# Kernel tuning notes

Hardware: AMD Instinct MI355X
Metric: run time of the kernel (lower is better)

The kernel has to match this reference:

```python
import jax, jax.numpy as jnp
import numpy as np
import math

B, T, D, H = 2, 2048, 1024, 16
HD = D // H  # head_dim = 64
ROPE_BASE = 10000.0


def _rope_tables(t_len, dim, base, dtype=jnp.float32):
    inv_freq = 1.0 / (base ** (jnp.arange(0, dim, 2, dtype=jnp.float32) / dim))
    t = jnp.arange(t_len, dtype=jnp.float32)
    freqs = jnp.outer(t, inv_freq)                 # [T, dim/2]
    emb = jnp.concatenate([freqs, freqs], axis=-1)  # [T, dim]
    return jnp.cos(emb).astype(dtype), jnp.sin(emb).astype(dtype)


def _rotate_half(x):
    x1, x2 = jnp.split(x, 2, axis=-1)
    return jnp.concatenate([-x2, x1], axis=-1)


def _apply_rotary(x, cos, sin):
    # x: [B,H,T,hd]; cos/sin: [T,hd] broadcast over B,H
    return x * cos[None, None, :, :] + _rotate_half(x) * sin[None, None, :, :]


def setup_inputs() -> dict:
    key = jax.random.key(0)
    ks = jax.random.split(key, 5)
    x = jax.random.normal(ks[0], (B, T, D), dtype=jnp.float32)
    Wq = jax.random.normal(ks[1], (D, D), dtype=jnp.float32) * (1.0 / math.sqrt(D))
    Wk = jax.random.normal(ks[2], (D, D), dtype=jnp.float32) * (1.0 / math.sqrt(D))
    Wv = jax.random.normal(ks[3], (D, D), dtype=jnp.float32) * (1.0 / math.sqrt(D))
    Wo = jax.random.normal(ks[4], (D, D), dtype=jnp.float32) * (1.0 / math.sqrt(D))
    # additive causal mask: 0 on/below diagonal, -inf above
    neg = jnp.finfo(jnp.float32).min
    mask = jnp.where(jnp.tril(jnp.ones((T, T), dtype=bool)), 0.0, neg).astype(jnp.float32)
    return {"x": x, "mask": mask, "Wq": Wq, "Wk": Wk, "Wv": Wv, "Wo": Wo}


def reference(x, mask, Wq, Wk, Wv, Wo):
    scale = math.sqrt(HD)
    # projections (nn.Linear: y = x @ W.T), split heads -> [B,H,T,hd]
    q = jnp.einsum('btd,ed->bte', x, Wq).reshape(B, T, H, HD).transpose(0, 2, 1, 3)
    k = jnp.einsum('btd,ed->bte', x, Wk).reshape(B, T, H, HD).transpose(0, 2, 1, 3)
    v = jnp.einsum('btd,ed->bte', x, Wv).reshape(B, T, H, HD).transpose(0, 2, 1, 3)
    cos, sin = _rope_tables(T, HD, ROPE_BASE, x.dtype)
    q = _apply_rotary(q, cos, sin)
    k = _apply_rotary(k, cos, sin)
    scores = jnp.einsum('bhqd,bhkd->bhqk', q, k) / scale   # [B,H,T,T]
    scores = scores + mask[None, None, :, :]
    attn_weights = jax.nn.softmax(scores, axis=-1)          # [B,H,T,T]
    # dropout=0.0 (eval): attn_weights_dropped == attn_weights
    out = jnp.einsum('bhqk,bhkd->bhqd', attn_weights, v)    # [B,H,T,hd]
    out = out.transpose(0, 2, 1, 3).reshape(B, T, D)
    out = jnp.einsum('btd,ed->bte', out, Wo)
    return out, attn_weights
```

## Files before the change

### kernel.cpp

```cpp
#include <hip/hip_runtime.h>
#include <math.h>

#define Tn 2048
#define Dn 1024
#define Hn 16
#define HDn 64

typedef float f32x4 __attribute__((ext_vector_type(4)));
typedef _Float16 f16x8 __attribute__((ext_vector_type(8)));
typedef _Float16 f16x4 __attribute__((ext_vector_type(4)));
typedef __fp16 fp16x2 __attribute__((ext_vector_type(2)));

__device__ __forceinline__ f32x4 mfma16(f16x8 a, f16x8 b, f32x4 c) {
  return __builtin_amdgcn_mfma_f32_16x16x32_f16(a, b, c, 0, 0, 0);
}

__device__ __forceinline__ void cvt_store4(_Float16* dst, float4 v) {
  union { _Float16 h[4]; uint2 u; } pk;
  pk.h[0] = (_Float16)v.x; pk.h[1] = (_Float16)v.y;
  pk.h[2] = (_Float16)v.z; pk.h[3] = (_Float16)v.w;
  *reinterpret_cast<uint2*>(dst) = pk.u;
}

__device__ __forceinline__ void nt_store4v(float* p, f32x4 t) {
  __builtin_nontemporal_store(t, reinterpret_cast<f32x4*>(p));
}

__device__ __forceinline__ f16x4 pk4(float a, float b, float c, float d) {
  union { fp16x2 v[2]; f16x4 h; } u;
  u.v[0] = __builtin_amdgcn_cvt_pkrtz(a, b);
  u.v[1] = __builtin_amdgcn_cvt_pkrtz(c, d);
  return u.h;
}

#define SOFT_SYNC do {                                        \
    __builtin_amdgcn_sched_barrier(0);                        \
    asm volatile("s_waitcnt lgkmcnt(0)" ::: "memory");        \
    __builtin_amdgcn_s_barrier();                             \
    __builtin_amdgcn_sched_barrier(0);                        \
  } while (0)

__global__ __launch_bounds__(256) void cvt_fp16_kernel(
    const float* __restrict__ x, const float* __restrict__ wq,
    const float* __restrict__ wk, const float* __restrict__ wv,
    const float* __restrict__ wo,
    _Float16* __restrict__ xh, _Float16* __restrict__ wqh,
    _Float16* __restrict__ wkh, _Float16* __restrict__ wvh,
    _Float16* __restrict__ woh)
{
  int i = blockIdx.x * 256 + threadIdx.x;
  const float* src; _Float16* dst; int off;
  if (i < 1048576) { src = x; dst = xh; off = i; }
  else {
    int j = i - 1048576;
    int w = j >> 18; off = j & 262143;
    src = (w == 0) ? wq : (w == 1) ? wk : (w == 2) ? wv : wo;
    dst = (w == 0) ? wqh : (w == 1) ? wkh : (w == 2) ? wvh : woh;
  }
  float4 v = reinterpret_cast<const float4*>(src)[off];
  cvt_store4(dst + (size_t)off * 4, v);
}

__global__ void rope_table_kernel(float* __restrict__ cosT, float* __restrict__ sinT) {
  int i = blockIdx.x * 256 + threadIdx.x;
  if (i >= Tn * 32) return;
  int t = i >> 5, f = i & 31;
  float inv = powf(10000.0f, -(float)(2 * f) / 64.0f);
  float ang = (float)t * inv;
  float c = cosf(ang), s = sinf(ang);
  cosT[t * HDn + f] = c; cosT[t * HDn + f + 32] = c;
  sinT[t * HDn + f] = s; sinT[t * HDn + f + 32] = s;
}

__global__ __launch_bounds__(256) void proj_kernel(
    const _Float16* __restrict__ xh, const _Float16* __restrict__ wqh,
    const _Float16* __restrict__ wkh, const _Float16* __restrict__ wvh,
    const float* __restrict__ cosT, const float* __restrict__ sinT,
    _Float16* __restrict__ qh, _Float16* __restrict__ kh, _Float16* __restrict__ vh)
{
  const int w = blockIdx.z;
  const _Float16* __restrict__ W = (w == 0) ? wqh : (w == 1) ? wkh : wvh;
  _Float16* __restrict__ dst = (w == 0) ? qh : (w == 1) ? kh : vh;
  __shared__ _Float16 As[128][72];
  __shared__ _Float16 Bs[128][72];
  const int tid = threadIdx.x;
  const int lane = tid & 63, wave = tid >> 6;
  const int lrow = lane & 15, lhi = lane >> 4;
  const int wm = wave >> 1, wn = wave & 1;
  const int m0 = blockIdx.x * 128, n0 = blockIdx.y * 128;
  f32x4 acc[4][4];
#pragma unroll
  for (int i = 0; i < 4; ++i)
#pragma unroll
    for (int j = 0; j < 4; ++j) acc[i][j] = f32x4{0.f, 0.f, 0.f, 0.f};

  for (int k0 = 0; k0 < Dn; k0 += 64) {
#pragma unroll
    for (int it = 0; it < 4; ++it) {
      int idx = it * 2048 + tid * 8;
      int r = idx >> 6, c = idx & 63;
      *reinterpret_cast<uint4*>(&As[r][c]) =
          *reinterpret_cast<const uint4*>(xh + (size_t)(m0 + r) * Dn + k0 + c);
      *reinterpret_cast<uint4*>(&Bs[r][c]) =
          *reinterpret_cast<const uint4*>(W + (size_t)(n0 + r) * Dn + k0 + c);
    }
    __syncthreads();
#pragma unroll
    for (int kc = 0; kc < 2; ++kc) {
      f16x8 af[4], bf[4];
#pragma unroll
      for (int i = 0; i < 4; ++i)
        af[i] = *reinterpret_cast<const f16x8*>(&As[wm * 64 + i * 16 + lrow][kc * 32 + lhi * 8]);
#pragma unroll
      for (int j = 0; j < 4; ++j)
        bf[j] = *reinterpret_cast<const f16x8*>(&Bs[wn * 64 + j * 16 + lrow][kc * 32 + lhi * 8]);
#pragma unroll
      for (int i = 0; i < 4; ++i)
#pragma unroll
        for (int j = 0; j < 4; ++j)
          acc[i][j] = mfma16(af[i], bf[j], acc[i][j]);
    }
    __syncthreads();
  }
  const bool isqk = (w < 2);
#pragma unroll
  for (int i = 0; i < 4; ++i) {
#pragma unroll
    for (int r = 0; r < 4; ++r) {
      int rowg = m0 + wm * 64 + i * 16 + lhi * 4 + r;
      int bb = rowg >> 11, t = rowg & (Tn - 1);
#pragma unroll
      for (int j = 0; j < 4; ++j) {
        int colg = n0 + wn * 64 + j * 16 + lrow;
        int hh = colg >> 6, d = colg & 63;
        float val = acc[i][j][r];
        if (isqk) {
          float partner = acc[i][j ^ 2][r];
          float rot = (j < 2) ? -partner : partner;
          val = val * cosT[t * HDn + d] + rot * sinT[t * HDn + d];
        }
        dst[(((size_t)(bb * Hn + hh)) * Tn + t) * HDn + d] = (_Float16)val;
      }
    }
  }
}

__global__ __launch_bounds__(256) void attn_kernel(
    const _Float16* __restrict__ qh, const _Float16* __restrict__ kh,
    const _Float16* __restrict__ vh, float* __restrict__ attnw,
    _Float16* __restrict__ obuf)
{
  const int f = blockIdx.x;
  const int s = f >> 3, g = s >> 5;
  const int my_bh = (f & 7) + 8 * g;
  const int c = ((s & 31) + 8 * g) & 31;
  const int b = my_bh >> 4, h = my_bh & 15;
  const size_t bh = (size_t)my_bh;
  const _Float16* __restrict__ Qp = qh + bh * Tn * HDn;
  const _Float16* __restrict__ Kp = kh + bh * Tn * HDn;
  const _Float16* __restrict__ Vp = vh + bh * Tn * HDn;
  float* __restrict__ attnp = attnw + bh * (size_t)Tn * Tn;

  __shared__ _Float16 Ks[128][72];
  __shared__ _Float16 Vt[64][136];
  __shared__ _Float16 Pt[4][16][136];

  const int tid = threadIdx.x;
  const int lane = tid & 63, wave = tid >> 6;
  const int q16 = lane & 15, lhi = lane >> 4;
  const int qp0 = c * 64;
  const int wrow = qp0 + wave * 16;
  const int qg = wrow + q16;
  const int ntiles = (c >> 1) + 1;

  f16x8 bq[2];
#pragma unroll
  for (int kc = 0; kc < 2; ++kc) {
    bq[kc] = *reinterpret_cast<const f16x8*>(
        Qp + (size_t)qg * HDn + kc * 32 + lhi * 8);
    bq[kc] = bq[kc] * (_Float16)0.18033688f;
  }

  float lsum = 0.f;
  for (int kt = 0; kt < ntiles; ++kt) {
#pragma unroll
    for (int it = 0; it < 4; ++it) {
      int idx = it * 2048 + tid * 8;
      int r = idx >> 6, cc = idx & 63;
      *reinterpret_cast<uint4*>(&Ks[r][cc]) =
          *reinterpret_cast<const uint4*>(Kp + (size_t)(kt * 128 + r) * HDn + cc);
    }
    SOFT_SYNC;
    f32x4 st[8];
#pragma unroll
    for (int nf = 0; nf < 8; ++nf) st[nf] = f32x4{0.f, 0.f, 0.f, 0.f};
#pragma unroll
    for (int kc = 0; kc < 2; ++kc) {
      f16x8 ak[8];
#pragma unroll
      for (int nf = 0; nf < 8; ++nf)
        ak[nf] = *reinterpret_cast<const f16x8*>(&Ks[nf * 16 + q16][kc * 32 + lhi * 8]);
#pragma unroll
      for (int nf = 0; nf < 8; ++nf) st[nf] = mfma16(ak[nf], bq[kc], st[nf]);
    }
    const bool diag = (kt == ntiles - 1);
#pragma unroll
    for (int nf = 0; nf < 8; ++nf) {
      int kbase = kt * 128 + nf * 16 + lhi * 4;
#pragma unroll
      for (int r = 0; r < 4; ++r) {
        float v = st[nf][r];
        if (diag && (kbase + r) > qg) v = -INFINITY;
        lsum += __builtin_amdgcn_exp2f(v);
      }
    }
    SOFT_SYNC;
  }
  lsum += __shfl_xor(lsum, 16);
  lsum += __shfl_xor(lsum, 32);
  const float lg = __builtin_amdgcn_logf(lsum);

  f32x4 oacc[4];
#pragma unroll
  for (int df = 0; df < 4; ++df) oacc[df] = f32x4{0.f, 0.f, 0.f, 0.f};

  for (int kt = 0; kt < ntiles; ++kt) {
#pragma unroll
    for (int it = 0; it < 4; ++it) {
      int idx = it * 2048 + tid * 8;
      int r = idx >> 6, cc = idx & 63;
      *reinterpret_cast<uint4*>(&Ks[r][cc]) =
          *reinterpret_cast<const uint4*>(Kp + (size_t)(kt * 128 + r) * HDn + cc);
      uint4 vv = *reinterpret_cast<const uint4*>(Vp + (size_t)(kt * 128 + r) * HDn + cc);
      const _Float16* pv = reinterpret_cast<const _Float16*>(&vv);
      int colb = ((((r >> 3) ^ (cc >> 3)) & 15) << 3) | (r & 7);
#pragma unroll
      for (int j = 0; j < 8; ++j) Vt[cc + j][colb] = pv[j];
    }
    SOFT_SYNC;
    f32x4 st[8];
#pragma unroll
    for (int nf = 0; nf < 8; ++nf) st[nf] = f32x4{0.f, 0.f, 0.f, 0.f};
#pragma unroll
    for (int kc = 0; kc < 2; ++kc) {
      f16x8 ak[8];
#pragma unroll
      for (int nf = 0; nf < 8; ++nf)
        ak[nf] = *reinterpret_cast<const f16x8*>(&Ks[nf * 16 + q16][kc * 32 + lhi * 8]);
#pragma unroll
      for (int nf = 0; nf < 8; ++nf) st[nf] = mfma16(ak[nf], bq[kc], st[nf]);
    }
    const bool diag = (kt == ntiles - 1);
#pragma unroll
    for (int nf = 0; nf < 8; ++nf) {
      int kbase = kt * 128 + nf * 16 + lhi * 4;
      float p[4];
#pragma unroll
      for (int r = 0; r < 4; ++r) {
        float v = st[nf][r];
        if (diag && (kbase + r) > qg) v = -INFINITY;
        p[r] = __builtin_amdgcn_exp2f(v - lg);
      }
      *reinterpret_cast<f16x4*>(&Pt[wave][q16][nf * 16 + lhi * 4]) =
          pk4(p[0], p[1], p[2], p[3]);
    }
#pragma unroll
    for (int kc2 = 0; kc2 < 4; ++kc2) {
      f16x8 ap = *reinterpret_cast<const f16x8*>(&Pt[wave][q16][kc2 * 32 + lhi * 8]);
      f16x8 bv[4];
#pragma unroll
      for (int df = 0; df < 4; ++df) {
        int d = df * 16 + q16;
        int colb = (((4 * kc2 + lhi) ^ ((d >> 3) & 7)) & 15) << 3;
        bv[df] = *reinterpret_cast<const f16x8*>(&Vt[d][colb]);
      }
#pragma unroll
      for (int df = 0; df < 4; ++df) oacc[df] = mfma16(ap, bv[df], oacc[df]);
    }
    {
      const int qrd = (lane >> 5);
      const int k4 = (lane & 31) * 4;
#pragma unroll
      for (int it2 = 0; it2 < 8; ++it2) {
        int qrow = it2 * 2 + qrd;
        f16x4 ph = *reinterpret_cast<const f16x4*>(&Pt[wave][qrow][k4]);
        f32x4 pf;
        pf[0] = (float)ph[0]; pf[1] = (float)ph[1];
        pf[2] = (float)ph[2]; pf[3] = (float)ph[3];
        nt_store4v(attnp + (size_t)(wrow + qrow) * Tn + kt * 128 + k4, pf);
      }
    }
    SOFT_SYNC;
  }

#pragma unroll
  for (int df = 0; df < 4; ++df)
#pragma unroll
    for (int r = 0; r < 4; ++r)
      obuf[((size_t)(b * Tn + wrow + lhi * 4 + r)) * Dn + h * HDn + df * 16 + q16] =
          (_Float16)oacc[df][r];

  int zc0 = ntiles * 128;
  if (zc0 < Tn) {
    int n4 = (Tn - zc0) >> 2;
    int total = 64 * n4;
    for (int i = tid; i < total; i += 256) {
      int r = i / n4, cc = (i - r * n4) * 4;
      f32x4 z = f32x4{0.f, 0.f, 0.f, 0.f};
      nt_store4v(attnp + (size_t)(qp0 + r) * Tn + zc0 + cc, z);
    }
  }
}

__global__ __launch_bounds__(256) void outproj_kernel(
    const _Float16* __restrict__ obuf, const _Float16* __restrict__ woh,
    float* __restrict__ out)
{
  __shared__ _Float16 As[128][72];
  __shared__ _Float16 Bs[128][72];
  const int tid = threadIdx.x;
  const int lane = tid & 63, wave = tid >> 6;
  const int lrow = lane & 15, lhi = lane >> 4;
  const int wm = wave >> 1, wn = wave & 1;
  const int m0 = blockIdx.x * 128, n0 = blockIdx.y * 128;
  f32x4 acc[4][4];
#pragma unroll
  for (int i = 0; i < 4; ++i)
#pragma unroll
    for (int j = 0; j < 4; ++j) acc[i][j] = f32x4{0.f, 0.f, 0.f, 0.f};

  for (int k0 = 0; k0 < Dn; k0 += 64) {
#pragma unroll
    for (int it = 0; it < 4; ++it) {
      int idx = it * 2048 + tid * 8;
      int r = idx >> 6, c = idx & 63;
      *reinterpret_cast<uint4*>(&As[r][c]) =
          *reinterpret_cast<const uint4*>(obuf + (size_t)(m0 + r) * Dn + k0 + c);
      *reinterpret_cast<uint4*>(&Bs[r][c]) =
          *reinterpret_cast<const uint4*>(woh + (size_t)(n0 + r) * Dn + k0 + c);
    }
    __syncthreads();
#pragma unroll
    for (int kc = 0; kc < 2; ++kc) {
      f16x8 af[4], bf[4];
#pragma unroll
      for (int i = 0; i < 4; ++i)
        af[i] = *reinterpret_cast<const f16x8*>(&As[wm * 64 + i * 16 + lrow][kc * 32 + lhi * 8]);
#pragma unroll
      for (int j = 0; j < 4; ++j)
        bf[j] = *reinterpret_cast<const f16x8*>(&Bs[wn * 64 + j * 16 + lrow][kc * 32 + lhi * 8]);
#pragma unroll
      for (int i = 0; i < 4; ++i)
#pragma unroll
        for (int j = 0; j < 4; ++j)
          acc[i][j] = mfma16(af[i], bf[j], acc[i][j]);
    }
    __syncthreads();
  }
#pragma unroll
  for (int i = 0; i < 4; ++i)
#pragma unroll
    for (int j = 0; j < 4; ++j)
#pragma unroll
      for (int r = 0; r < 4; ++r) {
        int rowg = m0 + wm * 64 + i * 16 + lhi * 4 + r;
        int colg = n0 + wn * 64 + j * 16 + lrow;
        out[(size_t)rowg * Dn + colg] = acc[i][j][r];
      }
}

extern "C" void kernel_launch(void* const* d_in, const int* in_sizes, int n_in,
                              void* d_out, int out_size, void* d_ws, size_t ws_size,
                              hipStream_t stream) {
  const float* x  = (const float*)d_in[0];
  const float* Wq = (const float*)d_in[2];
  const float* Wk = (const float*)d_in[3];
  const float* Wv = (const float*)d_in[4];
  const float* Wo = (const float*)d_in[5];

  float* out   = (float*)d_out;
  float* attnw = out + (size_t)2 * Tn * Dn;

  char* ws = (char*)d_ws;
  float* cosT = (float*)ws;
  float* sinT = cosT + Tn * HDn;
  _Float16* xh   = (_Float16*)(sinT + Tn * HDn);
  _Float16* obuf = xh;
  _Float16* wqh  = xh + (size_t)2 * Tn * Dn;
  _Float16* wkh  = wqh + Dn * Dn;
  _Float16* wvh  = wkh + Dn * Dn;
  _Float16* woh  = wvh + Dn * Dn;
  _Float16* qh   = woh + Dn * Dn;
  _Float16* kh   = qh + (size_t)2 * Tn * Dn;
  _Float16* vh   = kh + (size_t)2 * Tn * Dn;

  cvt_fp16_kernel<<<dim3(8192), 256, 0, stream>>>(x, Wq, Wk, Wv, Wo,
                                                  xh, wqh, wkh, wvh, woh);
  rope_table_kernel<<<dim3(256), 256, 0, stream>>>(cosT, sinT);
  proj_kernel<<<dim3(32, 8, 3), 256, 0, stream>>>(xh, wqh, wkh, wvh,
                                                  cosT, sinT, qh, kh, vh);
  attn_kernel<<<dim3(1024), 256, 0, stream>>>(qh, kh, vh, attnw, obuf);
  outproj_kernel<<<dim3(32, 8, 1), 256, 0, stream>>>(obuf, woh, out);
}
```

Baseline: 224.3 us.

## Prefetch next K/V tiles into registers during attention compute

```diff
diff --git a/kernel.cpp b/kernel.cpp
--- a/kernel.cpp
+++ b/kernel.cpp
@@ -173,6 +173,9 @@
   const int qg = wrow + q16;
   const int ntiles = (c >> 1) + 1;
 
+  const int sr0 = (tid * 8) >> 6;
+  const int scc = (tid * 8) & 63;
+
   f16x8 bq[2];
 #pragma unroll
   for (int kc = 0; kc < 2; ++kc) {
@@ -182,14 +185,17 @@
   }
 
   float lsum = 0.f;
+  uint4 kreg[4];
+#pragma unroll
+  for (int it = 0; it < 4; ++it)
+    kreg[it] = *reinterpret_cast<const uint4*>(
+        Vp != Kp ? Kp + (size_t)(sr0 + it * 32) * HDn + scc
+                 : Kp + (size_t)(sr0 + it * 32) * HDn + scc);
   for (int kt = 0; kt < ntiles; ++kt) {
-#pragma unroll
-    for (int it = 0; it < 4; ++it) {
-      int idx = it * 2048 + tid * 8;
-      int r = idx >> 6, cc = idx & 63;
-      *reinterpret_cast<uint4*>(&Ks[r][cc]) =
-          *reinterpret_cast<const uint4*>(Kp + (size_t)(kt * 128 + r) * HDn + cc);
-    }
+    SOFT_SYNC;
+#pragma unroll
+    for (int it = 0; it < 4; ++it)
+      *reinterpret_cast<uint4*>(&Ks[sr0 + it * 32][scc]) = kreg[it];
     SOFT_SYNC;
     f32x4 st[8];
 #pragma unroll
@@ -202,6 +208,12 @@
         ak[nf] = *reinterpret_cast<const f16x8*>(&Ks[nf * 16 + q16][kc * 32 + lhi * 8]);
 #pragma unroll
       for (int nf = 0; nf < 8; ++nf) st[nf] = mfma16(ak[nf], bq[kc], st[nf]);
+    }
+    if (kt + 1 < ntiles) {
+#pragma unroll
+      for (int it = 0; it < 4; ++it)
+        kreg[it] = *reinterpret_cast<const uint4*>(
+            Kp + (size_t)((kt + 1) * 128 + sr0 + it * 32) * HDn + scc);
     }
     const bool diag = (kt == ntiles - 1);
 #pragma unroll
@@ -214,7 +226,6 @@
         lsum += __builtin_amdgcn_exp2f(v);
       }
     }
-    SOFT_SYNC;
   }
   lsum += __shfl_xor(lsum, 16);
   lsum += __shfl_xor(lsum, 32);
@@ -224,18 +235,23 @@
 #pragma unroll
   for (int df = 0; df < 4; ++df) oacc[df] = f32x4{0.f, 0.f, 0.f, 0.f};
 
+  uint4 vreg[4];
+#pragma unroll
+  for (int it = 0; it < 4; ++it) {
+    kreg[it] = *reinterpret_cast<const uint4*>(Kp + (size_t)(sr0 + it * 32) * HDn + scc);
+    vreg[it] = *reinterpret_cast<const uint4*>(Vp + (size_t)(sr0 + it * 32) * HDn + scc);
+  }
+
   for (int kt = 0; kt < ntiles; ++kt) {
+    SOFT_SYNC;
 #pragma unroll
     for (int it = 0; it < 4; ++it) {
-      int idx = it * 2048 + tid * 8;
-      int r = idx >> 6, cc = idx & 63;
-      *reinterpret_cast<uint4*>(&Ks[r][cc]) =
-          *reinterpret_cast<const uint4*>(Kp + (size_t)(kt * 128 + r) * HDn + cc);
-      uint4 vv = *reinterpret_cast<const uint4*>(Vp + (size_t)(kt * 128 + r) * HDn + cc);
-      const _Float16* pv = reinterpret_cast<const _Float16*>(&vv);
-      int colb = ((((r >> 3) ^ (cc >> 3)) & 15) << 3) | (r & 7);
-#pragma unroll
-      for (int j = 0; j < 8; ++j) Vt[cc + j][colb] = pv[j];
+      int r = sr0 + it * 32;
+      *reinterpret_cast<uint4*>(&Ks[r][scc]) = kreg[it];
+      const _Float16* pv = reinterpret_cast<const _Float16*>(&vreg[it]);
+      int colb = ((((r >> 3) ^ (scc >> 3)) & 15) << 3) | (r & 7);
+#pragma unroll
+      for (int j = 0; j < 8; ++j) Vt[scc + j][colb] = pv[j];
     }
     SOFT_SYNC;
     f32x4 st[8];
@@ -277,6 +293,16 @@
 #pragma unroll
       for (int df = 0; df < 4; ++df) oacc[df] = mfma16(ap, bv[df], oacc[df]);
     }
+    if (kt + 1 < ntiles) {
+#pragma unroll
+      for (int it = 0; it < 4; ++it) {
+        kreg[it] = *reinterpret_cast<const uint4*>(
+            Kp + (size_t)((kt + 1) * 128 + sr0 + it * 32) * HDn + scc);
+        vreg[it] = *reinterpret_cast<const uint4*>(
+            Vp + (size_t)((kt + 1) * 128 + sr0 + it * 32) * HDn + scc);
+      }
+    }
+    __builtin_amdgcn_sched_barrier(0);
     {
       const int qrd = (lane >> 5);
       const int k4 = (lane & 31) * 4;
@@ -290,7 +316,6 @@
         nt_store4v(attnp + (size_t)(wrow + qrow) * Tn + kt * 128 + k4, pf);
       }
     }
-    SOFT_SYNC;
   }
 
 #pragma unroll
```

New measurement: 274.1 us. +22.2%, slower.
